# Optimization experiments

Measured on AMD Instinct MI355X. Metric: run time of the kernel, lower is better.

Reference implementation:

```python
import jax, jax.numpy as jnp
import numpy as np

N, E, F, H, O, R = 50000, 600000, 128, 128, 64, 8


def setup_inputs() -> dict:
    key = jax.random.key(0)
    ks = jax.random.split(key, 10)
    x = jax.random.normal(ks[0], (N, F), dtype=jnp.float32)
    edge_index = jax.random.randint(ks[1], (2, E), 0, N, dtype=jnp.int64)
    edge_weight = jax.random.uniform(ks[2], (E,), dtype=jnp.float32)
    edge_type = jax.random.randint(ks[3], (E,), 0, R, dtype=jnp.int64)
    s = 1.0 / np.sqrt(F)
    W1 = jax.random.uniform(ks[4], (R, F, H), jnp.float32, -s, s)
    root1 = jax.random.uniform(ks[5], (F, H), jnp.float32, -s, s)
    bias1 = jnp.zeros((H,), jnp.float32)
    sh = 1.0 / np.sqrt(H)
    W2 = jax.random.uniform(ks[6], (R, H, O), jnp.float32, -sh, sh)
    root2 = jax.random.uniform(ks[7], (H, O), jnp.float32, -sh, sh)
    bias2 = jnp.zeros((O,), jnp.float32)
    return {"x": x, "edge_index": edge_index, "edge_weight": edge_weight,
            "edge_type": edge_type, "W1": W1, "root1": root1, "bias1": bias1,
            "W2": W2, "root2": root2, "bias2": bias2}


def _rgcn_conv(x, src, dst, et, ew, W, root, bias, num_nodes):
    # project every node by every relation: [N, R, out] (cheaper than per-edge
    # materialization of weight[edge_type] which is E x in x out)
    proj = jnp.einsum('nd,rdo->nro', x, W)
    # per-edge message = x_j @ W[edge_type] * edge_weight  -> [E, out]
    msg = proj[src, et] * ew[:, None]
    # weighted scatter-mean over destination nodes
    agg = jax.ops.segment_sum(msg, dst, num_segments=num_nodes)
    cnt = jax.ops.segment_sum(jnp.ones_like(ew), dst, num_segments=num_nodes)
    agg = agg / jnp.maximum(cnt, 1.0)[:, None]
    # root (self) transform + bias
    return agg + x @ root + bias


def reference(x, edge_index, edge_weight, edge_type, W1, root1, bias1, W2, root2, bias2):
    src, dst = edge_index[0], edge_index[1]
    et = edge_type.astype(jnp.int32)
    # min-max normalize edge weights as in RGCN.forward
    ew = (edge_weight - edge_weight.min()) / (edge_weight.max() - edge_weight.min() + 1e-8)
    n = x.shape[0]
    h = jax.nn.relu(_rgcn_conv(x, src, dst, et, ew, W1, root1, bias1, n))
    return _rgcn_conv(h, src, dst, et, ew, W2, root2, bias2, n)
```

## Files before the change

### kernel.cpp

```cpp
#include <hip/hip_runtime.h>

#define F_DIM 128
#define H_DIM 128
#define O_DIM 64
#define R_NUM 8

typedef __attribute__((ext_vector_type(8))) short bf16x8;
typedef __attribute__((ext_vector_type(4))) float f32x4;
typedef __attribute__((ext_vector_type(8))) unsigned short u16x8;

union V8 { bf16x8 v; short4 h[2]; };

__device__ __forceinline__ unsigned short f2b(float f) {
    unsigned u = __float_as_uint(f);
    u += 0x7FFFu + ((u >> 16) & 1u);
    return (unsigned short)(u >> 16);
}
__device__ __forceinline__ float b2f(unsigned short b) {
    return __uint_as_float(((unsigned)b) << 16);
}

__global__ __launch_bounds__(256) void setupA(
    const float* __restrict__ ew, const int* __restrict__ dst,
    const int* __restrict__ et, int E, int* __restrict__ deg2,
    float* __restrict__ bmn, float* __restrict__ bmx,
    const float* __restrict__ x, unsigned short* __restrict__ xb, long x4,
    const float* __restrict__ W1, const float* __restrict__ root1,
    const float* __restrict__ W2, const float* __restrict__ root2,
    unsigned short* __restrict__ wt1, unsigned short* __restrict__ wt2) {
    __shared__ float smn[256], smx[256];
    const int tid = threadIdx.x;
    const int gstride = gridDim.x * blockDim.x;
    int g0 = blockIdx.x * blockDim.x + tid;

    float mn = 1e30f, mx = -1e30f;
    for (int i = g0; i < E; i += gstride) {
        atomicAdd(&deg2[dst[i] * R_NUM + et[i]], 1);
        float v = ew[i];
        mn = fminf(mn, v);
        mx = fmaxf(mx, v);
    }
    smn[tid] = mn; smx[tid] = mx;
    __syncthreads();
    for (int s = 128; s > 0; s >>= 1) {
        if (tid < s) {
            smn[tid] = fminf(smn[tid], smn[tid + s]);
            smx[tid] = fmaxf(smx[tid], smx[tid + s]);
        }
        __syncthreads();
    }
    if (tid == 0) { bmn[blockIdx.x] = smn[0]; bmx[blockIdx.x] = smx[0]; }

    for (long i = g0; i < x4; i += gstride) {
        float4 v = ((const float4*)x)[i];
        ushort4 o;
        o.x = f2b(v.x); o.y = f2b(v.y); o.z = f2b(v.z); o.w = f2b(v.w);
        ((ushort4*)xb)[i] = o;
    }

    const int n1 = 9 * 128 * 128, n2 = 9 * 64 * 128;
    for (int idx = g0; idx < n1 + n2; idx += gstride) {
        if (idx < n1) {
            int r = idx / (128 * 128), rem = idx % (128 * 128);
            int n = rem / 128, k = rem % 128;
            float v = (r < 8) ? W1[((size_t)r * 128 + k) * 128 + n]
                              : root1[(size_t)k * 128 + n];
            wt1[idx] = f2b(v);
        } else {
            int j = idx - n1;
            int r = j / (64 * 128), rem = j % (64 * 128);
            int n = rem / 128, k = rem % 128;
            float v = (r < 8) ? W2[((size_t)r * 128 + k) * 64 + n]
                              : root2[(size_t)k * 64 + n];
            wt2[j] = f2b(v);
        }
    }
}

__global__ void scan1_kernel(const int* __restrict__ deg, int* __restrict__ rp,
                             int* __restrict__ bsum, float* __restrict__ invc,
                             int M, int N) {
    __shared__ int s[256];
    int base = blockIdx.x * 2048;
    int t = threadIdx.x;
    int v[8]; int loc = 0;
#pragma unroll
    for (int i = 0; i < 8; ++i) {
        int idx = base + t * 8 + i;
        v[i] = (idx < M) ? deg[idx] : 0;
        loc += v[i];
    }
    int node = blockIdx.x * 256 + t;
    if (node < N) invc[node] = 1.0f / (float)max(loc, 1);
    s[t] = loc;
    __syncthreads();
    for (int off = 1; off < 256; off <<= 1) {
        int x = (t >= off) ? s[t - off] : 0;
        __syncthreads();
        s[t] += x;
        __syncthreads();
    }
    int run = s[t] - loc;
#pragma unroll
    for (int i = 0; i < 8; ++i) {
        int idx = base + t * 8 + i;
        if (idx < M) rp[idx] = run;
        run += v[i];
    }
    if (t == 255) bsum[blockIdx.x] = s[255];
}

__global__ void scan2_mm(int* bsum, int nb, const float* __restrict__ bmn,
                         const float* __restrict__ bmx, float* mm) {
    __shared__ int s[256];
    __shared__ float smn[256], smx[256];
    int t = threadIdx.x;
    int v = (t < nb) ? bsum[t] : 0;
    s[t] = v;
    smn[t] = fminf(bmn[t], bmn[t + 256]);
    smx[t] = fmaxf(bmx[t], bmx[t + 256]);
    __syncthreads();
    for (int off = 1; off < 256; off <<= 1) {
        int x = (t >= off) ? s[t - off] : 0;
        __syncthreads();
        s[t] += x;
        __syncthreads();
    }
    if (t < nb) bsum[t] = s[t] - v;
    for (int r = 128; r > 0; r >>= 1) {
        if (t < r) {
            smn[t] = fminf(smn[t], smn[t + r]);
            smx[t] = fmaxf(smx[t], smx[t + r]);
        }
        __syncthreads();
    }
    if (t == 0) { mm[0] = smn[0]; mm[1] = smx[0]; }
}

__global__ void fill2_kernel(const int* __restrict__ src, const int* __restrict__ dst,
                             const int* __restrict__ et, const float* __restrict__ ew,
                             const float* __restrict__ mm, const float* __restrict__ invc,
                             int* __restrict__ rp2, const int* __restrict__ bsum,
                             unsigned* __restrict__ erec, int E) {
    int e = blockIdx.x * blockDim.x + threadIdx.x;
    if (e >= E) return;
    int d = dst[e];
    int i = d * R_NUM + et[e];
    int pos = atomicAdd(&rp2[i], 1) + bsum[i >> 11];
    float mn = mm[0], mx = mm[1];
    unsigned wq = f2b((ew[e] - mn) / (mx - mn + 1e-8f) * invc[d]);
    erec[pos] = (wq << 17) | (unsigned)src[e];
}

__global__ __launch_bounds__(256) void gather_y(
    const int* __restrict__ rp2, const int* __restrict__ bsum,
    const unsigned* __restrict__ erec,
    const unsigned short* __restrict__ inp,
    unsigned short* __restrict__ y, int N) {
    int gid = blockIdx.x * 256 + threadIdx.x;
    int seg = gid >> 4;
    int n = seg >> 3;
    if (n >= N) return;
    int j = (gid & 15) * 8;
    int beg = (seg == 0) ? 0 : rp2[seg - 1] + bsum[(seg - 1) >> 11];
    int end = rp2[seg] + bsum[seg >> 11];
    float acc[8] = {0.f, 0.f, 0.f, 0.f, 0.f, 0.f, 0.f, 0.f};
    int k = beg;
    for (; k + 2 <= end; k += 2) {
        unsigned r0 = erec[k], r1 = erec[k + 1];
        float w0 = __uint_as_float((r0 >> 1) & 0x7FFF8000u);
        float w1 = __uint_as_float((r1 >> 1) & 0x7FFF8000u);
        u16x8 v0 = *(const u16x8*)(inp + (size_t)(r0 & 0x1FFFFu) * 128 + j);
        u16x8 v1 = *(const u16x8*)(inp + (size_t)(r1 & 0x1FFFFu) * 128 + j);
#pragma unroll
        for (int c = 0; c < 8; ++c) acc[c] += w0 * b2f(v0[c]);
#pragma unroll
        for (int c = 0; c < 8; ++c) acc[c] += w1 * b2f(v1[c]);
    }
    if (k < end) {
        unsigned r0 = erec[k];
        float w0 = __uint_as_float((r0 >> 1) & 0x7FFF8000u);
        u16x8 v0 = *(const u16x8*)(inp + (size_t)(r0 & 0x1FFFFu) * 128 + j);
#pragma unroll
        for (int c = 0; c < 8; ++c) acc[c] += w0 * b2f(v0[c]);
    }
    u16x8 o;
#pragma unroll
    for (int c = 0; c < 8; ++c) o[c] = f2b(acc[c]);
    *(u16x8*)(y + (size_t)seg * 128 + j) = o;
}

template <int NCOL, bool RELU>
__global__ __launch_bounds__(256) void gemm_y(
    const unsigned short* __restrict__ y,
    const unsigned short* __restrict__ inp,
    const unsigned short* __restrict__ Wt,
    const float* __restrict__ bias,
    unsigned short* __restrict__ outb, int N)
{
    constexpr int NT = NCOL / 16;
    __shared__ unsigned short smem[64 * 132 + NCOL * 132];
    unsigned short* ys  = smem;
    unsigned short* wsd = smem + 64 * 132;

    const int tid = threadIdx.x;
    const int w = tid >> 6, lane = tid & 63;
    const int quad = lane >> 4, l15 = lane & 15;
    const int n0 = blockIdx.x * 64;

    f32x4 acc[NT];
#pragma unroll
    for (int nt = 0; nt < NT; ++nt) acc[nt] = (f32x4){0.f, 0.f, 0.f, 0.f};

    for (int r = 0; r < 9; ++r) {
#pragma unroll
        for (int it = 0; it < NCOL / 16; ++it) {
            int u = tid + it * 256;
            int row = u >> 4, seg = u & 15;
            V8 v;
            v.v = *(const bf16x8*)(Wt + ((size_t)r * NCOL + row) * 128 + seg * 8);
            *(short4*)&wsd[row * 132 + seg * 8]     = v.h[0];
            *(short4*)&wsd[row * 132 + seg * 8 + 4] = v.h[1];
        }
#pragma unroll
        for (int it = 0; it < 4; ++it) {
            int u = tid + it * 256;
            int row = u >> 4, seg = u & 15;
            int node = n0 + row;
            if (node >= N) node = N - 1;
            const unsigned short* src = (r < 8)
                ? y + ((size_t)node * R_NUM + r) * 128 + seg * 8
                : inp + (size_t)node * 128 + seg * 8;
            V8 v; v.v = *(const bf16x8*)src;
            *(short4*)&ys[row * 132 + seg * 8]     = v.h[0];
            *(short4*)&ys[row * 132 + seg * 8 + 4] = v.h[1];
        }
        __syncthreads();
        const unsigned short* yrow = ys + (size_t)(w * 16 + l15) * 132 + quad * 8;
#pragma unroll
        for (int k2 = 0; k2 < 4; ++k2) {
            V8 b;
            b.h[0] = *(const short4*)(yrow + k2 * 32);
            b.h[1] = *(const short4*)(yrow + k2 * 32 + 4);
#pragma unroll
            for (int nt = 0; nt < NT; ++nt) {
                const unsigned short* ar = wsd + (size_t)(nt * 16 + l15) * 132
                                           + k2 * 32 + quad * 8;
                V8 av;
                av.h[0] = *(const short4*)ar;
                av.h[1] = *(const short4*)(ar + 4);
                acc[nt] = __builtin_amdgcn_mfma_f32_16x16x32_bf16(av.v, b.v, acc[nt], 0, 0, 0);
            }
        }
        __syncthreads();
    }

    const int gn = tid >> 2, gq = tid & 3;
    const int gnode = n0 + gn;
    unsigned short* stg = smem;
#pragma unroll
    for (int nt = 0; nt < NT; ++nt) {
        int c0 = nt * 16 + quad * 4;
        float4 bs = *(const float4*)(bias + c0);
        float v0 = acc[nt][0] + bs.x, v1 = acc[nt][1] + bs.y;
        float v2 = acc[nt][2] + bs.z, v3 = acc[nt][3] + bs.w;
        if (RELU) {
            v0 = fmaxf(v0, 0.f); v1 = fmaxf(v1, 0.f);
            v2 = fmaxf(v2, 0.f); v3 = fmaxf(v3, 0.f);
        }
        short4 o;
        o.x = (short)f2b(v0); o.y = (short)f2b(v1);
        o.z = (short)f2b(v2); o.w = (short)f2b(v3);
        *(short4*)&stg[(w * 16 + l15) * 136 + c0] = o;
    }
    __syncthreads();
    if (gnode < N) {
        const unsigned short* srw = stg + gn * 136 + gq * (NCOL / 4);
        unsigned short* drow = outb + (size_t)gnode * NCOL + gq * (NCOL / 4);
#pragma unroll
        for (int c = 0; c < NCOL / 32; ++c)
            *(bf16x8*)(drow + c * 8) = *(const bf16x8*)(srw + c * 8);
    }
}

__global__ __launch_bounds__(256) void gemm_proj2(
    const unsigned short* __restrict__ h,
    const unsigned short* __restrict__ Wt,
    unsigned short* __restrict__ proj2,
    int N)
{
    __shared__ unsigned short hs[64 * 132];
    __shared__ unsigned short wsd[64 * 132];
    __shared__ unsigned short ts[64 * 68];

    const int tid = threadIdx.x;
    const int w = tid >> 6, lane = tid & 63;
    const int quad = lane >> 4, l15 = lane & 15;
    const int n0 = blockIdx.x * 64;

#pragma unroll
    for (int it = 0; it < 4; ++it) {
        int u = tid + it * 256;
        int row = u >> 4, seg = u & 15;
        int node = n0 + row;
        if (node >= N) node = N - 1;
        V8 v; v.v = *(const bf16x8*)(h + (size_t)node * 128 + seg * 8);
        *(short4*)&hs[row * 132 + seg * 8]     = v.h[0];
        *(short4*)&hs[row * 132 + seg * 8 + 4] = v.h[1];
    }

    for (int r = 0; r < 9; ++r) {
#pragma unroll
        for (int it = 0; it < 4; ++it) {
            int u = tid + it * 256;
            int row = u >> 4, seg = u & 15;
            V8 v;
            v.v = *(const bf16x8*)(Wt + ((size_t)r * 64 + row) * 128 + seg * 8);
            *(short4*)&wsd[row * 132 + seg * 8]     = v.h[0];
            *(short4*)&wsd[row * 132 + seg * 8 + 4] = v.h[1];
        }
        __syncthreads();
        f32x4 acc[4];
#pragma unroll
        for (int nt = 0; nt < 4; ++nt) acc[nt] = (f32x4){0.f, 0.f, 0.f, 0.f};
        const unsigned short* yrow = hs + (size_t)(w * 16 + l15) * 132 + quad * 8;
#pragma unroll
        for (int k2 = 0; k2 < 4; ++k2) {
            V8 b;
            b.h[0] = *(const short4*)(yrow + k2 * 32);
            b.h[1] = *(const short4*)(yrow + k2 * 32 + 4);
#pragma unroll
            for (int nt = 0; nt < 4; ++nt) {
                const unsigned short* ar = wsd + (size_t)(nt * 16 + l15) * 132
                                           + k2 * 32 + quad * 8;
                V8 av;
                av.h[0] = *(const short4*)ar;
                av.h[1] = *(const short4*)(ar + 4);
                acc[nt] = __builtin_amdgcn_mfma_f32_16x16x32_bf16(av.v, b.v, acc[nt], 0, 0, 0);
            }
        }
        unsigned short* tw = ts + w * 16 * 68;
#pragma unroll
        for (int nt = 0; nt < 4; ++nt) {
            int c0 = nt * 16 + quad * 4;
            short4 o;
            o.x = (short)f2b(acc[nt][0]); o.y = (short)f2b(acc[nt][1]);
            o.z = (short)f2b(acc[nt][2]); o.w = (short)f2b(acc[nt][3]);
            *(short4*)&tw[l15 * 68 + c0] = o;
        }
#pragma unroll
        for (int jj = 0; jj < 2; ++jj) {
            int rl = (lane >> 3) + 8 * jj;
            int off = (lane & 7) * 8;
            int g = n0 + w * 16 + rl;
            V8 v;
            v.h[0] = *(const short4*)&tw[rl * 68 + off];
            v.h[1] = *(const short4*)&tw[rl * 68 + off + 4];
            if (g < N)
                *(bf16x8*)(proj2 + ((size_t)r * N + g) * 64 + off) = v.v;
        }
        __syncthreads();
    }
}

__global__ __launch_bounds__(256) void gather_out2(
    const int* __restrict__ rp2, const int* __restrict__ bsum,
    const unsigned* __restrict__ erec,
    const unsigned short* __restrict__ proj2,
    const float* __restrict__ bias,
    float* __restrict__ out, int N)
{
    int gid = blockIdx.x * 256 + threadIdx.x;
    int n = gid >> 3;
    if (n >= N) return;
    int j = (gid & 7) * 8;

    int base = n * R_NUM;
    int bs_n = bsum[base >> 11];
    int4 ea = *(const int4*)(rp2 + base);
    int4 eb = *(const int4*)(rp2 + base + 4);
    int ends[8] = {ea.x + bs_n, ea.y + bs_n, ea.z + bs_n, ea.w + bs_n,
                   eb.x + bs_n, eb.y + bs_n, eb.z + bs_n, eb.w + bs_n};
    int k = (n == 0) ? 0 : rp2[base - 1] + bsum[(base - 1) >> 11];

    float acc[8] = {0.f, 0.f, 0.f, 0.f, 0.f, 0.f, 0.f, 0.f};
#pragma unroll
    for (int r = 0; r < 8; ++r) {
        int end = ends[r];
        for (; k < end; ++k) {
            unsigned rec = erec[k];
            float wgt = __uint_as_float((rec >> 1) & 0x7FFF8000u);
            u16x8 v = *(const u16x8*)(proj2 + ((size_t)r * N + (rec & 0x1FFFFu)) * 64 + j);
#pragma unroll
            for (int c = 0; c < 8; ++c) acc[c] += wgt * b2f(v[c]);
        }
    }
    u16x8 sv = *(const u16x8*)(proj2 + ((size_t)8 * N + n) * 64 + j);
    float4 b0 = *(const float4*)(bias + j);
    float4 b1 = *(const float4*)(bias + j + 4);
    float* o = out + (size_t)n * 64 + j;
    o[0] = acc[0] + b2f(sv[0]) + b0.x;
    o[1] = acc[1] + b2f(sv[1]) + b0.y;
    o[2] = acc[2] + b2f(sv[2]) + b0.z;
    o[3] = acc[3] + b2f(sv[3]) + b0.w;
    o[4] = acc[4] + b2f(sv[4]) + b1.x;
    o[5] = acc[5] + b2f(sv[5]) + b1.y;
    o[6] = acc[6] + b2f(sv[6]) + b1.z;
    o[7] = acc[7] + b2f(sv[7]) + b1.w;
}

extern "C" void kernel_launch(void* const* d_in, const int* in_sizes, int n_in,
                              void* d_out, int out_size, void* d_ws, size_t ws_size,
                              hipStream_t stream) {
    const float* x     = (const float*)d_in[0];
    const int*   ei    = (const int*)d_in[1];
    const float* ew    = (const float*)d_in[2];
    const int*   et    = (const int*)d_in[3];
    const float* W1    = (const float*)d_in[4];
    const float* root1 = (const float*)d_in[5];
    const float* bias1 = (const float*)d_in[6];
    const float* W2    = (const float*)d_in[7];
    const float* root2 = (const float*)d_in[8];
    const float* bias2 = (const float*)d_in[9];

    const int N = in_sizes[0] / F_DIM;
    const int E = in_sizes[2];
    const int M2 = N * R_NUM;
    const int* srcp = ei;
    const int* dstp = ei + E;

    int* base = (int*)d_ws;
    float* mm    = (float*)base;
    float* invc  = (float*)(base + 16);
    int*   deg2  = base + 16 + N;
    int*   rp2   = deg2 + M2;
    int*   bsum  = rp2 + M2;
    float* bmn   = (float*)(bsum + 256);
    float* bmx   = bmn + 512;
    unsigned* erec = (unsigned*)(bmx + 512);
    unsigned short* xb  = (unsigned short*)(erec + E);
    unsigned short* hb  = xb + (size_t)N * 128;
    unsigned short* wt1 = hb + (size_t)N * 128;
    unsigned short* wt2 = wt1 + 9 * 128 * 128;
    unsigned short* y   = wt2 + 9 * 64 * 128;
    unsigned short* proj2 = y;

    const int TB = 256;
    int blocksE = (E + TB - 1) / TB;
    int nb = (M2 + 2047) / 2048;
    long x4 = (long)N * 128 / 4;

    hipMemsetAsync(deg2, 0, (size_t)M2 * sizeof(int), stream);
    setupA<<<512, TB, 0, stream>>>(ew, dstp, et, E, deg2, bmn, bmx,
                                   x, xb, x4, W1, root1, W2, root2, wt1, wt2);
    scan1_kernel<<<nb, TB, 0, stream>>>(deg2, rp2, bsum, invc, M2, N);
    scan2_mm<<<1, TB, 0, stream>>>(bsum, nb, bmn, bmx, mm);
    fill2_kernel<<<blocksE, TB, 0, stream>>>(srcp, dstp, et, ew, mm, invc,
                                             rp2, bsum, erec, E);

    int gatB = (int)(((long)M2 * 16 + TB - 1) / TB);
    int gB = (N + 63) / 64;

    gather_y<<<gatB, TB, 0, stream>>>(rp2, bsum, erec, xb, y, N);
    gemm_y<H_DIM, true><<<gB, TB, 0, stream>>>(y, xb, wt1, bias1, hb, N);

    gemm_proj2<<<gB, TB, 0, stream>>>(hb, wt2, proj2, N);
    int g2B = (int)(((long)N * 8 + TB - 1) / TB);
    gather_out2<<<g2B, TB, 0, stream>>>(rp2, bsum, erec, proj2, bias2,
                                        (float*)d_out, N);
}
```

Before: 299.5 us.

## Fuse layer-1 per-relation gather into the MFMA GEMM kernel

Removes the separate gather_y kernel and its N*R*128 bf16 intermediate buffer y. The gemm kernel now aggregates the weighted neighbour features for each relation directly into shared memory before running the MFMA step. This cuts a large global write and read round-trip, but the irregular gather now sits inside the GEMM loop with only 782 blocks. That gives less parallelism for hiding latency, and the weight tile loads are serialised behind the gather.

```diff
diff --git a/kernel.cpp b/kernel.cpp
--- a/kernel.cpp
+++ b/kernel.cpp
@@ -152,47 +152,10 @@
     erec[pos] = (wq << 17) | (unsigned)src[e];
 }
 
-__global__ __launch_bounds__(256) void gather_y(
+template <int NCOL, bool RELU>
+__global__ __launch_bounds__(256) void gemm_fused1(
     const int* __restrict__ rp2, const int* __restrict__ bsum,
     const unsigned* __restrict__ erec,
-    const unsigned short* __restrict__ inp,
-    unsigned short* __restrict__ y, int N) {
-    int gid = blockIdx.x * 256 + threadIdx.x;
-    int seg = gid >> 4;
-    int n = seg >> 3;
-    if (n >= N) return;
-    int j = (gid & 15) * 8;
-    int beg = (seg == 0) ? 0 : rp2[seg - 1] + bsum[(seg - 1) >> 11];
-    int end = rp2[seg] + bsum[seg >> 11];
-    float acc[8] = {0.f, 0.f, 0.f, 0.f, 0.f, 0.f, 0.f, 0.f};
-    int k = beg;
-    for (; k + 2 <= end; k += 2) {
-        unsigned r0 = erec[k], r1 = erec[k + 1];
-        float w0 = __uint_as_float((r0 >> 1) & 0x7FFF8000u);
-        float w1 = __uint_as_float((r1 >> 1) & 0x7FFF8000u);
-        u16x8 v0 = *(const u16x8*)(inp + (size_t)(r0 & 0x1FFFFu) * 128 + j);
-        u16x8 v1 = *(const u16x8*)(inp + (size_t)(r1 & 0x1FFFFu) * 128 + j);
-#pragma unroll
-        for (int c = 0; c < 8; ++c) acc[c] += w0 * b2f(v0[c]);
-#pragma unroll
-        for (int c = 0; c < 8; ++c) acc[c] += w1 * b2f(v1[c]);
-    }
-    if (k < end) {
-        unsigned r0 = erec[k];
-        float w0 = __uint_as_float((r0 >> 1) & 0x7FFF8000u);
-        u16x8 v0 = *(const u16x8*)(inp + (size_t)(r0 & 0x1FFFFu) * 128 + j);
-#pragma unroll
-        for (int c = 0; c < 8; ++c) acc[c] += w0 * b2f(v0[c]);
-    }
-    u16x8 o;
-#pragma unroll
-    for (int c = 0; c < 8; ++c) o[c] = f2b(acc[c]);
-    *(u16x8*)(y + (size_t)seg * 128 + j) = o;
-}
-
-template <int NCOL, bool RELU>
-__global__ __launch_bounds__(256) void gemm_y(
-    const unsigned short* __restrict__ y,
     const unsigned short* __restrict__ inp,
     const unsigned short* __restrict__ Wt,
     const float* __restrict__ bias,
@@ -207,6 +170,8 @@
     const int w = tid >> 6, lane = tid & 63;
     const int quad = lane >> 4, l15 = lane & 15;
     const int n0 = blockIdx.x * 64;
+    const int grp = tid >> 4;
+    const int j = (tid & 15) * 8;
 
     f32x4 acc[NT];
 #pragma unroll
@@ -222,18 +187,54 @@
             *(short4*)&wsd[row * 132 + seg * 8]     = v.h[0];
             *(short4*)&wsd[row * 132 + seg * 8 + 4] = v.h[1];
         }
-#pragma unroll
-        for (int it = 0; it < 4; ++it) {
-            int u = tid + it * 256;
-            int row = u >> 4, seg = u & 15;
-            int node = n0 + row;
-            if (node >= N) node = N - 1;
-            const unsigned short* src = (r < 8)
-                ? y + ((size_t)node * R_NUM + r) * 128 + seg * 8
-                : inp + (size_t)node * 128 + seg * 8;
-            V8 v; v.v = *(const bf16x8*)src;
-            *(short4*)&ys[row * 132 + seg * 8]     = v.h[0];
-            *(short4*)&ys[row * 132 + seg * 8 + 4] = v.h[1];
+        if (r < 8) {
+#pragma unroll
+            for (int g = 0; g < 4; ++g) {
+                int row = g * 16 + grp;
+                int node = n0 + row;
+                if (node >= N) node = N - 1;
+                int sg = node * R_NUM + r;
+                int beg = (sg == 0) ? 0 : rp2[sg - 1] + bsum[(sg - 1) >> 11];
+                int end = rp2[sg] + bsum[sg >> 11];
+                float ac[8] = {0.f, 0.f, 0.f, 0.f, 0.f, 0.f, 0.f, 0.f};
+                int k = beg;
+                for (; k + 2 <= end; k += 2) {
+                    unsigned r0 = erec[k], r1 = erec[k + 1];
+                    float w0 = __uint_as_float((r0 >> 1) & 0x7FFF8000u);
+                    float w1 = __uint_as_float((r1 >> 1) & 0x7FFF8000u);
+                    u16x8 v0 = *(const u16x8*)(inp + (size_t)(r0 & 0x1FFFFu) * 128 + j);
+                    u16x8 v1 = *(const u16x8*)(inp + (size_t)(r1 & 0x1FFFFu) * 128 + j);
+#pragma unroll
+                    for (int c = 0; c < 8; ++c) ac[c] += w0 * b2f(v0[c]);
+#pragma unroll
+                    for (int c = 0; c < 8; ++c) ac[c] += w1 * b2f(v1[c]);
+                }
+                if (k < end) {
+                    unsigned r0 = erec[k];
+                    float w0 = __uint_as_float((r0 >> 1) & 0x7FFF8000u);
+                    u16x8 v0 = *(const u16x8*)(inp + (size_t)(r0 & 0x1FFFFu) * 128 + j);
+#pragma unroll
+                    for (int c = 0; c < 8; ++c) ac[c] += w0 * b2f(v0[c]);
+                }
+                short4 h0, h1;
+                h0.x = (short)f2b(ac[0]); h0.y = (short)f2b(ac[1]);
+                h0.z = (short)f2b(ac[2]); h0.w = (short)f2b(ac[3]);
+                h1.x = (short)f2b(ac[4]); h1.y = (short)f2b(ac[5]);
+                h1.z = (short)f2b(ac[6]); h1.w = (short)f2b(ac[7]);
+                *(short4*)&ys[row * 132 + j]     = h0;
+                *(short4*)&ys[row * 132 + j + 4] = h1;
+            }
+        } else {
+#pragma unroll
+            for (int it = 0; it < 4; ++it) {
+                int u = tid + it * 256;
+                int row = u >> 4, seg = u & 15;
+                int node = n0 + row;
+                if (node >= N) node = N - 1;
+                V8 v; v.v = *(const bf16x8*)(inp + (size_t)node * 128 + seg * 8);
+                *(short4*)&ys[row * 132 + seg * 8]     = v.h[0];
+                *(short4*)&ys[row * 132 + seg * 8 + 4] = v.h[1];
+            }
         }
         __syncthreads();
         const unsigned short* yrow = ys + (size_t)(w * 16 + l15) * 132 + quad * 8;
@@ -442,8 +443,7 @@
     unsigned short* hb  = xb + (size_t)N * 128;
     unsigned short* wt1 = hb + (size_t)N * 128;
     unsigned short* wt2 = wt1 + 9 * 128 * 128;
-    unsigned short* y   = wt2 + 9 * 64 * 128;
-    unsigned short* proj2 = y;
+    unsigned short* proj2 = wt2 + 9 * 64 * 128;
 
     const int TB = 256;
     int blocksE = (E + TB - 1) / TB;
@@ -458,11 +458,10 @@
     fill2_kernel<<<blocksE, TB, 0, stream>>>(srcp, dstp, et, ew, mm, invc,
                                              rp2, bsum, erec, E);
 
-    int gatB = (int)(((long)M2 * 16 + TB - 1) / TB);
     int gB = (N + 63) / 64;
 
-    gather_y<<<gatB, TB, 0, stream>>>(rp2, bsum, erec, xb, y, N);
-    gemm_y<H_DIM, true><<<gB, TB, 0, stream>>>(y, xb, wt1, bias1, hb, N);
+    gemm_fused1<H_DIM, true><<<gB, TB, 0, stream>>>(rp2, bsum, erec, xb, wt1,
+                                                    bias1, hb, N);
 
     gemm_proj2<<<gB, TB, 0, stream>>>(hb, wt2, proj2, N);
     int g2B = (int)(((long)N * 8 + TB - 1) / TB);
```

New measurement: 360.8 us. 20.5% more time.

## Double-buffer layer-1 GEMM tiles and load weights directly into registers

Applied to the files above, without the earlier changes.

Rewrites the layer-1 aggregate GEMM so each wave loads its slice of the per-relation weight matrix straight from global memory into registers instead of staging it through shared memory. The aggregated-feature tile is double-buffered in LDS, with the next relation's tile prefetched into registers during the current MFMA work. One barrier per relation replaces two. Launch bounds of 3 blocks per CU are requested to raise occupancy. The trade-offs are repeated global or L2 weight reads per block and higher register pressure.

```diff
diff --git a/kernel.cpp b/kernel.cpp
--- a/kernel.cpp
+++ b/kernel.cpp
@@ -190,95 +190,112 @@
     *(u16x8*)(y + (size_t)seg * 128 + j) = o;
 }
 
-template <int NCOL, bool RELU>
-__global__ __launch_bounds__(256) void gemm_y(
+__global__ __launch_bounds__(256, 3) void gemm_y2(
     const unsigned short* __restrict__ y,
     const unsigned short* __restrict__ inp,
     const unsigned short* __restrict__ Wt,
     const float* __restrict__ bias,
     unsigned short* __restrict__ outb, int N)
 {
-    constexpr int NT = NCOL / 16;
-    __shared__ unsigned short smem[64 * 132 + NCOL * 132];
-    unsigned short* ys  = smem;
-    unsigned short* wsd = smem + 64 * 132;
+    __shared__ unsigned short smem[2 * 64 * 132];
 
     const int tid = threadIdx.x;
     const int w = tid >> 6, lane = tid & 63;
     const int quad = lane >> 4, l15 = lane & 15;
     const int n0 = blockIdx.x * 64;
 
-    f32x4 acc[NT];
-#pragma unroll
-    for (int nt = 0; nt < NT; ++nt) acc[nt] = (f32x4){0.f, 0.f, 0.f, 0.f};
-
-    for (int r = 0; r < 9; ++r) {
-#pragma unroll
-        for (int it = 0; it < NCOL / 16; ++it) {
-            int u = tid + it * 256;
-            int row = u >> 4, seg = u & 15;
-            V8 v;
-            v.v = *(const bf16x8*)(Wt + ((size_t)r * NCOL + row) * 128 + seg * 8);
-            *(short4*)&wsd[row * 132 + seg * 8]     = v.h[0];
-            *(short4*)&wsd[row * 132 + seg * 8 + 4] = v.h[1];
-        }
+    V8 st[4];
+    int srow[4], sseg[4];
+#pragma unroll
+    for (int it = 0; it < 4; ++it) {
+        int u = tid + it * 256;
+        srow[it] = u >> 4;
+        sseg[it] = u & 15;
+    }
+
+    auto issue = [&](int r) {
 #pragma unroll
         for (int it = 0; it < 4; ++it) {
-            int u = tid + it * 256;
-            int row = u >> 4, seg = u & 15;
-            int node = n0 + row;
+            int node = n0 + srow[it];
             if (node >= N) node = N - 1;
             const unsigned short* src = (r < 8)
-                ? y + ((size_t)node * R_NUM + r) * 128 + seg * 8
-                : inp + (size_t)node * 128 + seg * 8;
-            V8 v; v.v = *(const bf16x8*)src;
-            *(short4*)&ys[row * 132 + seg * 8]     = v.h[0];
-            *(short4*)&ys[row * 132 + seg * 8 + 4] = v.h[1];
-        }
-        __syncthreads();
-        const unsigned short* yrow = ys + (size_t)(w * 16 + l15) * 132 + quad * 8;
+                ? y + ((size_t)node * R_NUM + r) * 128 + sseg[it] * 8
+                : inp + (size_t)node * 128 + sseg[it] * 8;
+            st[it].v = *(const bf16x8*)src;
+        }
+    };
+
+    f32x4 acc[4][2];
+#pragma unroll
+    for (int g = 0; g < 4; ++g) {
+        acc[g][0] = (f32x4){0.f, 0.f, 0.f, 0.f};
+        acc[g][1] = (f32x4){0.f, 0.f, 0.f, 0.f};
+    }
+
+    issue(0);
+
+    for (int r = 0; r < 9; ++r) {
+        unsigned short* ysb = smem + (r & 1) * (64 * 132);
+#pragma unroll
+        for (int it = 0; it < 4; ++it) {
+            *(short4*)&ysb[srow[it] * 132 + sseg[it] * 8]     = st[it].h[0];
+            *(short4*)&ysb[srow[it] * 132 + sseg[it] * 8 + 4] = st[it].h[1];
+        }
+        if (r < 8) issue(r + 1);
+        asm volatile("s_waitcnt lgkmcnt(0)" ::: "memory");
+        __builtin_amdgcn_s_barrier();
+
+        const unsigned short* wbase = Wt + (size_t)r * 128 * 128;
+        bf16x8 afr[2][4];
 #pragma unroll
         for (int k2 = 0; k2 < 4; ++k2) {
-            V8 b;
-            b.h[0] = *(const short4*)(yrow + k2 * 32);
-            b.h[1] = *(const short4*)(yrow + k2 * 32 + 4);
-#pragma unroll
-            for (int nt = 0; nt < NT; ++nt) {
-                const unsigned short* ar = wsd + (size_t)(nt * 16 + l15) * 132
+#pragma unroll
+            for (int cc = 0; cc < 2; ++cc) {
+                afr[cc][k2] = *(const bf16x8*)(wbase
+                    + (size_t)((w * 2 + cc) * 16 + l15) * 128 + k2 * 32 + quad * 8);
+            }
+        }
+#pragma unroll
+        for (int k2 = 0; k2 < 4; ++k2) {
+#pragma unroll
+            for (int g = 0; g < 4; ++g) {
+                const unsigned short* yr = ysb + (size_t)(g * 16 + l15) * 132
                                            + k2 * 32 + quad * 8;
-                V8 av;
-                av.h[0] = *(const short4*)ar;
-                av.h[1] = *(const short4*)(ar + 4);
-                acc[nt] = __builtin_amdgcn_mfma_f32_16x16x32_bf16(av.v, b.v, acc[nt], 0, 0, 0);
+                V8 b;
+                b.h[0] = *(const short4*)yr;
+                b.h[1] = *(const short4*)(yr + 4);
+                acc[g][0] = __builtin_amdgcn_mfma_f32_16x16x32_bf16(afr[0][k2], b.v, acc[g][0], 0, 0, 0);
+                acc[g][1] = __builtin_amdgcn_mfma_f32_16x16x32_bf16(afr[1][k2], b.v, acc[g][1], 0, 0, 0);
             }
         }
-        __syncthreads();
-    }
-
+    }
+
+    __syncthreads();
+    unsigned short* stg = smem;
+#pragma unroll
+    for (int g = 0; g < 4; ++g) {
+#pragma unroll
+        for (int cc = 0; cc < 2; ++cc) {
+            int c0 = (w * 2 + cc) * 16 + quad * 4;
+            float4 bs = *(const float4*)(bias + c0);
+            float v0 = acc[g][cc][0] + bs.x, v1 = acc[g][cc][1] + bs.y;
+            float v2 = acc[g][cc][2] + bs.z, v3 = acc[g][cc][3] + bs.w;
+            v0 = fmaxf(v0, 0.f); v1 = fmaxf(v1, 0.f);
+            v2 = fmaxf(v2, 0.f); v3 = fmaxf(v3, 0.f);
+            short4 o;
+            o.x = (short)f2b(v0); o.y = (short)f2b(v1);
+            o.z = (short)f2b(v2); o.w = (short)f2b(v3);
+            *(short4*)&stg[(g * 16 + l15) * 136 + c0] = o;
+        }
+    }
+    __syncthreads();
     const int gn = tid >> 2, gq = tid & 3;
     const int gnode = n0 + gn;
-    unsigned short* stg = smem;
-#pragma unroll
-    for (int nt = 0; nt < NT; ++nt) {
-        int c0 = nt * 16 + quad * 4;
-        float4 bs = *(const float4*)(bias + c0);
-        float v0 = acc[nt][0] + bs.x, v1 = acc[nt][1] + bs.y;
-        float v2 = acc[nt][2] + bs.z, v3 = acc[nt][3] + bs.w;
-        if (RELU) {
-            v0 = fmaxf(v0, 0.f); v1 = fmaxf(v1, 0.f);
-            v2 = fmaxf(v2, 0.f); v3 = fmaxf(v3, 0.f);
-        }
-        short4 o;
-        o.x = (short)f2b(v0); o.y = (short)f2b(v1);
-        o.z = (short)f2b(v2); o.w = (short)f2b(v3);
-        *(short4*)&stg[(w * 16 + l15) * 136 + c0] = o;
-    }
-    __syncthreads();
     if (gnode < N) {
-        const unsigned short* srw = stg + gn * 136 + gq * (NCOL / 4);
-        unsigned short* drow = outb + (size_t)gnode * NCOL + gq * (NCOL / 4);
-#pragma unroll
-        for (int c = 0; c < NCOL / 32; ++c)
+        const unsigned short* srw = stg + gn * 136 + gq * 32;
+        unsigned short* drow = outb + (size_t)gnode * 128 + gq * 32;
+#pragma unroll
+        for (int c = 0; c < 4; ++c)
             *(bf16x8*)(drow + c * 8) = *(const bf16x8*)(srw + c * 8);
     }
 }
@@ -462,7 +479,7 @@
     int gB = (N + 63) / 64;
 
     gather_y<<<gatB, TB, 0, stream>>>(rp2, bsum, erec, xb, y, N);
-    gemm_y<H_DIM, true><<<gB, TB, 0, stream>>>(y, xb, wt1, bias1, hb, N);
+    gemm_y2<<<gB, TB, 0, stream>>>(y, xb, wt1, bias1, hb, N);
 
     gemm_proj2<<<gB, TB, 0, stream>>>(hb, wt2, proj2, N);
     int g2B = (int)(((long)N * 8 + TB - 1) / TB);
```

After: 302.0 us. No clear change (+0.8%).
